# Kernel optimization log

Hardware: AMD Instinct MI355X
Metric: run time of the kernel (lower is better)

Reference implementation:

```python
import jax, jax.numpy as jnp
import numpy as np


def _closest_dist_sum(p1, p2):
    # p1: [B, N, 3], p2: [B, M, 3]
    # Euclidean distance via the expanded quadratic form; matches
    # torch.norm(p1 - p2, 2, dim=3) -> min over p2 -> sum over all.
    d2 = (jnp.sum(p1 * p1, axis=-1)[:, :, None]
          + jnp.sum(p2 * p2, axis=-1)[:, None, :]
          - 2.0 * jnp.einsum('bnd,bmd->bnm', p1, p2))  # [B, N, M]
    d = jnp.sqrt(jnp.maximum(d2, 0.0))
    return jnp.sum(jnp.min(d, axis=2))


def setup_inputs() -> dict:
    key = jax.random.key(0)
    k1, k2 = jax.random.split(key)
    shape_xyz = jax.random.normal(k1, (8, 8192, 6), dtype=jnp.float32)
    skel_xyz = jax.random.normal(k2, (8, 2048, 3), dtype=jnp.float32)
    return {"shape_xyz": shape_xyz, "skel_xyz": skel_xyz}


def reference(shape_xyz, skel_xyz):
    # normals (shape_xyz[:, :, 3:6]) are extracted but unused in the loss
    pts = shape_xyz[:, :, :3]
    cd1 = _closest_dist_sum(pts, skel_xyz)   # shape -> skeleton
    cd2 = _closest_dist_sum(skel_xyz, pts)   # skeleton -> shape
    loss_cd = (cd1 + cd2) * 0.0001
    return loss_cd
```

## Files before the change

### kernel.cpp

```cpp
#include <hip/hip_runtime.h>

#define BATCH   8
#define SHAPE_N 8192
#define SKEL_M  2048
#define CHUNK   512

#define WS2_OFF 512
#define CNT_OFF 66048
#define RED_OFF 66056
#define SKC_OFF 66176
#define SHC_OFF (66176 + 131072)

typedef short bf16x8 __attribute__((ext_vector_type(8)));
typedef float f32x16 __attribute__((ext_vector_type(16)));
union FragU { bf16x8 v; uint4 u4; };

__device__ __forceinline__ unsigned int f2bf(float a) {
    unsigned int u = __float_as_uint(a);
    return (u + 0x7FFFu + ((u >> 16) & 1u)) >> 16;
}
__device__ __forceinline__ float bf2f(unsigned int h) {
    return __uint_as_float(h << 16);
}
__device__ __forceinline__ unsigned int pack2(unsigned int lo, unsigned int hi) {
    return lo | (hi << 16);
}
__device__ __forceinline__ void bfsplit(float v, unsigned int& h, unsigned int& l) {
    h = f2bf(v);
    l = f2bf(v - bf2f(h));
}

__device__ __forceinline__ void conv_point(float bx, float by, float bz,
                                           uint4& hi, uint4& lo) {
    const float cx = -2.f * bx, cy = -2.f * by, cz = -2.f * bz;
    const float rb = bx * bx + by * by + bz * bz;
    unsigned int chx, clx, chy, cly, chz, clz, rbh, rbl;
    bfsplit(cx, chx, clx); bfsplit(cy, chy, cly); bfsplit(cz, chz, clz);
    bfsplit(rb, rbh, rbl);
    hi = make_uint4(pack2(chx, chy), pack2(chz, rbh),
                    pack2(chx, chy), pack2(chz, rbl));
    lo = make_uint4(pack2(clx, cly), pack2(clz, 0u), 0u, 0u);
}

__device__ __forceinline__ void gl16(const char* g, char* l) {
    __builtin_amdgcn_global_load_lds(
        (const __attribute__((address_space(1))) void*)g,
        (__attribute__((address_space(3))) void*)l, 16, 0, 0);
}

__global__ __launch_bounds__(256) void cd_prep(
    const float* __restrict__ shape, const float* __restrict__ skel,
    float* __restrict__ ws)
{
    if (blockIdx.x == 0 && threadIdx.x == 0)
        ((int*)ws)[CNT_OFF] = 0;

    const int p = blockIdx.x * 256 + threadIdx.x;
    const float* q;
    uint4* dst;
    int idx;
    if (p < BATCH * SKEL_M) {
        const int b = p >> 11; idx = p & (SKEL_M - 1);
        q = skel + (size_t)p * 3;
        dst = (uint4*)(ws + SKC_OFF) + (size_t)b * 4096;
    } else {
        const int s = p - BATCH * SKEL_M;
        const int b = s >> 13; idx = s & (SHAPE_N - 1);
        q = shape + (size_t)s * 6;
        dst = (uint4*)(ws + SHC_OFF) + (size_t)b * 16384;
    }
    uint4 hi, lo;
    conv_point(q[0], q[1], q[2], hi, lo);
    const int g = idx >> 5, r = idx & 31;
    dst[g * 64 + r]      = hi;
    dst[g * 64 + 32 + r] = lo;
}

template <int SA>
__device__ __forceinline__ void cd_scan2(
    const float* __restrict__ Araw,
    const uint4* __restrict__ Bconv,
    uint4* __restrict__ sB,
    float* rmin, float* ra)
{
    const int tid = threadIdx.x;
    const int l = tid & 63, wv = tid >> 6;
    const unsigned int one = 0x3F80u;

    FragU bf[4];
#pragma unroll
    for (int j = 0; j < 4; ++j) {
        const float* p = Araw + (size_t)(j * 32 + (l & 31)) * SA;
        const float x = p[0], y = p[1], z = p[2];
        ra[j] = x * x + y * y + z * z;
        unsigned int hx, lx, hy, ly, hz, lz;
        bfsplit(x, hx, lx); bfsplit(y, hy, ly); bfsplit(z, hz, lz);
        if (l < 32)
            bf[j].u4 = make_uint4(pack2(hx, hy), pack2(hz, one),
                                  pack2(lx, ly), pack2(lz, one));
        else
            bf[j].u4 = make_uint4(pack2(hx, hy), pack2(hz, 0u), 0u, 0u);
        rmin[j] = 3.4e38f;
    }

    const f32x16 Z = {0,0,0,0,0,0,0,0,0,0,0,0,0,0,0,0};
    const char* gbase = (const char*)Bconv;
    char* lbase = (char*)sB;

#pragma unroll
    for (int k = 0; k < 4; ++k)
        gl16(gbase + k * 4096 + tid * 16, lbase + k * 4096 + tid * 16);
    __syncthreads();

    for (int c = 0; c < 4; ++c) {
        if (c < 3) {
            const char* src = gbase + (size_t)(c + 1) * 16384;
            char* dstl = lbase + (((c + 1) & 1) ? 16384 : 0);
#pragma unroll
            for (int k = 0; k < 4; ++k)
                gl16(src + k * 4096 + tid * 16, dstl + k * 4096 + tid * 16);
        }
        unsigned int o = (unsigned int)(((c & 1) ? 16384 : 0) + wv * 4096 +
                                        (l >> 5) * 512 + (l & 31) * 16);
#pragma unroll
        for (int g = 0; g < 4; ++g) {
            FragU af;
            af.u4 = *(const uint4*)(lbase + o);
            o += 1024;
#pragma unroll
            for (int j = 0; j < 4; ++j) {
                f32x16 D = __builtin_amdgcn_mfma_f32_32x32x16_bf16(
                    af.v, bf[j].v, Z, 0, 0, 0);
                const float t0 = fminf(fminf(D[0],  D[1]),  D[2]);
                const float t1 = fminf(fminf(D[3],  D[4]),  D[5]);
                const float t2 = fminf(fminf(D[6],  D[7]),  D[8]);
                const float t3 = fminf(fminf(D[9],  D[10]), D[11]);
                const float t4 = fminf(fminf(D[12], D[13]), D[14]);
                const float u0 = fminf(fminf(t0, t1), t2);
                const float u1 = fminf(fminf(t3, t4), D[15]);
                rmin[j] = fminf(rmin[j], fminf(u0, u1));
            }
        }
        __syncthreads();
    }
#pragma unroll
    for (int j = 0; j < 4; ++j)
        rmin[j] = fminf(rmin[j], __shfl_xor(rmin[j], 32, 64));
}

__global__ __launch_bounds__(256, 4) void cd_main(
    const float* __restrict__ shape, const float* __restrict__ skel,
    float* __restrict__ ws)
{
    __shared__ uint4 sB[CHUNK * 4];
    __shared__ float smin[4][128];
    __shared__ float sra[128];
    __shared__ float s_wsum[2];
    const int tid = threadIdx.x;
    const int l = tid & 63, wv = tid >> 6;
    const int bid = blockIdx.x;
    float rmin[4], ra[4];

    if (bid < 512) {
        const int b = bid >> 6, sub = bid & 63;
        cd_scan2<6>(shape + ((size_t)b * SHAPE_N + sub * 128) * 6,
                    (const uint4*)(ws + SKC_OFF) + (size_t)b * 4096,
                    sB, rmin, ra);
    } else {
        const int j = bid - 512;
        const int b = j >> 6, rem = j & 63;
        const int asub = rem >> 2, bs = rem & 3;
        cd_scan2<3>(skel + ((size_t)b * SKEL_M + asub * 128) * 3,
                    (const uint4*)(ws + SHC_OFF) + (size_t)b * 16384 + bs * 4096,
                    sB, rmin, ra);
    }

    if (l < 32) {
#pragma unroll
        for (int j = 0; j < 4; ++j) smin[wv][j * 32 + l] = rmin[j];
        if (wv == 0) {
#pragma unroll
            for (int j = 0; j < 4; ++j) sra[j * 32 + l] = ra[j];
        }
    }
    __syncthreads();

    if (bid < 512) {
        float d = 0.f;
        if (tid < 128) {
            const float m = fminf(fminf(smin[0][tid], smin[1][tid]),
                                  fminf(smin[2][tid], smin[3][tid]));
            d = sqrtf(fmaxf(sra[tid] + m, 0.f));
        }
        for (int o = 32; o; o >>= 1) d += __shfl_down(d, o, 64);
        if (l == 0 && wv < 2) s_wsum[wv] = d;
        __syncthreads();
        if (tid == 0) ws[bid] = s_wsum[0] + s_wsum[1];
    } else {
        if (tid < 128) {
            const int j = bid - 512;
            const int b = j >> 6, rem = j & 63;
            const int asub = rem >> 2, bs = rem & 3;
            const float m = fminf(fminf(smin[0][tid], smin[1][tid]),
                                  fminf(smin[2][tid], smin[3][tid]));
            ws[WS2_OFF + bs * (BATCH * SKEL_M) + b * SKEL_M +
               asub * 128 + tid] = sra[tid] + m;
        }
    }
}

__global__ __launch_bounds__(256) void cd_reduce(
    float* __restrict__ ws, float* __restrict__ out)
{
    __shared__ float s_wsum[4];
    __shared__ int s_last;
    const int t = threadIdx.x;
    const int bid = blockIdx.x;
    const int l = t & 63, wv = t >> 6;
    const int i = bid * 256 + t;

    const float v0 = ws[WS2_OFF + i];
    const float v1 = ws[WS2_OFF + 16384 + i];
    const float v2 = ws[WS2_OFF + 32768 + i];
    const float v3 = ws[WS2_OFF + 49152 + i];
    float s = sqrtf(fmaxf(fminf(fminf(v0, v1), fminf(v2, v3)), 0.f));
    if (bid < 2) s += ws[bid * 256 + t];

    for (int o = 32; o; o >>= 1) s += __shfl_down(s, o, 64);
    if (l == 0) s_wsum[wv] = s;
    __syncthreads();
    if (t == 0) {
        ws[RED_OFF + bid] = s_wsum[0] + s_wsum[1] + s_wsum[2] + s_wsum[3];
        __threadfence();
        const int old = atomicAdd((int*)ws + CNT_OFF, 1);
        s_last = (old == 63);
    }
    __syncthreads();
    if (s_last && wv == 0) {
        __threadfence();
        float f = ws[RED_OFF + l];
        for (int o = 32; o; o >>= 1) f += __shfl_down(f, o, 64);
        if (l == 0) out[0] = f * 1e-4f;
    }
}

extern "C" void kernel_launch(void* const* d_in, const int* in_sizes, int n_in,
                              void* d_out, int out_size, void* d_ws, size_t ws_size,
                              hipStream_t stream) {
    const float* shape = (const float*)d_in[0];
    const float* skel  = (const float*)d_in[1];
    float* out         = (float*)d_out;
    float* ws          = (float*)d_ws;

    cd_prep<<<320, 256, 0, stream>>>(shape, skel, ws);
    cd_main<<<1024, 256, 0, stream>>>(shape, skel, ws);
    cd_reduce<<<64, 256, 0, stream>>>(ws, out);
}
```

Baseline: 73.95 us.

## Load B fragments directly from global into registers, dropping LDS staging

Removes the LDS double-buffer staging (global_load_lds plus __syncthreads) of the converted B points. Each wave now reads its own contiguous 16 KB slice straight from global memory into registers, with an 8-deep software prefetch ring feeding the MFMA-and-min loop. This eliminates block-level barriers and the 32 KB of shared memory, which may raise occupancy. In exchange, the hiding of global latency now rests on register prefetch and cache hits rather than on a cooperative LDS load.

```diff
diff --git a/kernel.cpp b/kernel.cpp
--- a/kernel.cpp
+++ b/kernel.cpp
@@ -3,7 +3,6 @@
 #define BATCH   8
 #define SHAPE_N 8192
 #define SKEL_M  2048
-#define CHUNK   512
 
 #define WS2_OFF 512
 #define CNT_OFF 66048
@@ -40,12 +39,6 @@
     hi = make_uint4(pack2(chx, chy), pack2(chz, rbh),
                     pack2(chx, chy), pack2(chz, rbl));
     lo = make_uint4(pack2(clx, cly), pack2(clz, 0u), 0u, 0u);
-}
-
-__device__ __forceinline__ void gl16(const char* g, char* l) {
-    __builtin_amdgcn_global_load_lds(
-        (const __attribute__((address_space(1))) void*)g,
-        (__attribute__((address_space(3))) void*)l, 16, 0, 0);
 }
 
 __global__ __launch_bounds__(256) void cd_prep(
@@ -76,11 +69,29 @@
     dst[g * 64 + 32 + r] = lo;
 }
 
+__device__ __forceinline__ void step_min(const FragU& af, const FragU* bf,
+                                         float* rmin)
+{
+    const f32x16 Z = {0,0,0,0,0,0,0,0,0,0,0,0,0,0,0,0};
+#pragma unroll
+    for (int j = 0; j < 4; ++j) {
+        f32x16 D = __builtin_amdgcn_mfma_f32_32x32x16_bf16(
+            af.v, bf[j].v, Z, 0, 0, 0);
+        const float t0 = fminf(fminf(D[0],  D[1]),  D[2]);
+        const float t1 = fminf(fminf(D[3],  D[4]),  D[5]);
+        const float t2 = fminf(fminf(D[6],  D[7]),  D[8]);
+        const float t3 = fminf(fminf(D[9],  D[10]), D[11]);
+        const float t4 = fminf(fminf(D[12], D[13]), D[14]);
+        const float u0 = fminf(fminf(t0, t1), t2);
+        const float u1 = fminf(fminf(t3, t4), D[15]);
+        rmin[j] = fminf(rmin[j], fminf(u0, u1));
+    }
+}
+
 template <int SA>
 __device__ __forceinline__ void cd_scan2(
     const float* __restrict__ Araw,
     const uint4* __restrict__ Bconv,
-    uint4* __restrict__ sB,
     float* rmin, float* ra)
 {
     const int tid = threadIdx.x;
@@ -103,46 +114,23 @@
         rmin[j] = 3.4e38f;
     }
 
-    const f32x16 Z = {0,0,0,0,0,0,0,0,0,0,0,0,0,0,0,0};
-    const char* gbase = (const char*)Bconv;
-    char* lbase = (char*)sB;
-
-#pragma unroll
-    for (int k = 0; k < 4; ++k)
-        gl16(gbase + k * 4096 + tid * 16, lbase + k * 4096 + tid * 16);
-    __syncthreads();
-
-    for (int c = 0; c < 4; ++c) {
-        if (c < 3) {
-            const char* src = gbase + (size_t)(c + 1) * 16384;
-            char* dstl = lbase + (((c + 1) & 1) ? 16384 : 0);
-#pragma unroll
-            for (int k = 0; k < 4; ++k)
-                gl16(src + k * 4096 + tid * 16, dstl + k * 4096 + tid * 16);
-        }
-        unsigned int o = (unsigned int)(((c & 1) ? 16384 : 0) + wv * 4096 +
-                                        (l >> 5) * 512 + (l & 31) * 16);
-#pragma unroll
-        for (int g = 0; g < 4; ++g) {
-            FragU af;
-            af.u4 = *(const uint4*)(lbase + o);
-            o += 1024;
-#pragma unroll
-            for (int j = 0; j < 4; ++j) {
-                f32x16 D = __builtin_amdgcn_mfma_f32_32x32x16_bf16(
-                    af.v, bf[j].v, Z, 0, 0, 0);
-                const float t0 = fminf(fminf(D[0],  D[1]),  D[2]);
-                const float t1 = fminf(fminf(D[3],  D[4]),  D[5]);
-                const float t2 = fminf(fminf(D[6],  D[7]),  D[8]);
-                const float t3 = fminf(fminf(D[9],  D[10]), D[11]);
-                const float t4 = fminf(fminf(D[12], D[13]), D[14]);
-                const float u0 = fminf(fminf(t0, t1), t2);
-                const float u1 = fminf(fminf(t3, t4), D[15]);
-                rmin[j] = fminf(rmin[j], fminf(u0, u1));
-            }
-        }
-        __syncthreads();
-    }
+    const char* p0 = (const char*)Bconv + wv * 16384 +
+                     (l >> 5) * 512 + (l & 31) * 16;
+
+    FragU f[8];
+#pragma unroll
+    for (int g = 0; g < 8; ++g)
+        f[g].u4 = *(const uint4*)(p0 + g * 1024);
+#pragma unroll
+    for (int g = 0; g < 8; ++g) {
+        const FragU cur = f[g];
+        f[g].u4 = *(const uint4*)(p0 + (g + 8) * 1024);
+        step_min(cur, bf, rmin);
+    }
+#pragma unroll
+    for (int g = 0; g < 8; ++g)
+        step_min(f[g], bf, rmin);
+
 #pragma unroll
     for (int j = 0; j < 4; ++j)
         rmin[j] = fminf(rmin[j], __shfl_xor(rmin[j], 32, 64));
@@ -152,7 +140,6 @@
     const float* __restrict__ shape, const float* __restrict__ skel,
     float* __restrict__ ws)
 {
-    __shared__ uint4 sB[CHUNK * 4];
     __shared__ float smin[4][128];
     __shared__ float sra[128];
     __shared__ float s_wsum[2];
@@ -165,14 +152,14 @@
         const int b = bid >> 6, sub = bid & 63;
         cd_scan2<6>(shape + ((size_t)b * SHAPE_N + sub * 128) * 6,
                     (const uint4*)(ws + SKC_OFF) + (size_t)b * 4096,
-                    sB, rmin, ra);
+                    rmin, ra);
     } else {
         const int j = bid - 512;
         const int b = j >> 6, rem = j & 63;
         const int asub = rem >> 2, bs = rem & 3;
         cd_scan2<3>(skel + ((size_t)b * SKEL_M + asub * 128) * 3,
                     (const uint4*)(ws + SHC_OFF) + (size_t)b * 16384 + bs * 4096,
-                    sB, rmin, ra);
+                    rmin, ra);
     }
 
     if (l < 32) {
```

Result: no change. 72.61 us (-1.8%).
